# Performance work log

Hardware: AMD Instinct MI355X
Metric: run time of the kernel (lower is better)

## Reference

```python
import jax, jax.numpy as jnp
import numpy as np

DIM = 256      # dim_hidden * 2
HEADS = 8      # hier_tf_head
C = 256        # out_channels per head (concat=False)
FF = 1024      # dim_hidden * 8
N_HOPS = 4096
HOP_LEN = 12
N_MEM = N_HOPS * HOP_LEN
N = N_HOPS + N_MEM  # 53248 total nodes


def setup_inputs() -> dict:
    key = jax.random.key(0)
    ks = jax.random.split(key, 8)
    x = jax.random.normal(ks[0], (N, DIM), jnp.float32)
    # hop_attn structure built by the python loops: [j,j] self-edges for hop
    # tokens, then one edge (member_node -> hop_token) per member.
    hop_self = np.stack([np.arange(N_HOPS), np.arange(N_HOPS)])
    mem_src = np.arange(N_HOPS, N)
    mem_dst = np.arange(N_MEM) // HOP_LEN
    edge_index = jnp.asarray(
        np.concatenate([hop_self, np.stack([mem_src, mem_dst])], axis=1),
        jnp.int32)  # [2, E]

    def init(k, shp, fan):
        return jax.random.normal(k, shp, jnp.float32) / np.sqrt(fan).astype(np.float32)

    return {
        "x": x,
        "edge_index": edge_index,
        "gat_W": init(ks[1], (DIM, HEADS * C), DIM),
        "gat_att_src": init(ks[2], (HEADS, C), C),
        "gat_att_dst": init(ks[3], (HEADS, C), C),
        "gat_bias": jnp.zeros((C,), jnp.float32),
        "ffn_W1": init(ks[4], (DIM, FF), DIM),
        "ffn_b1": jnp.zeros((FF,), jnp.float32),
        "ffn_W2": init(ks[5], (FF, DIM), FF),
        "ffn_b2": jnp.zeros((DIM,), jnp.float32),
        "ln1_g": jnp.ones((DIM,), jnp.float32),
        "ln1_b": jnp.zeros((DIM,), jnp.float32),
        "ln2_g": jnp.ones((DIM,), jnp.float32),
        "ln2_b": jnp.zeros((DIM,), jnp.float32),
    }


def _layer_norm(x, g, b, eps=1e-5):
    mu = jnp.mean(x, axis=-1, keepdims=True)
    var = jnp.mean(jnp.square(x - mu), axis=-1, keepdims=True)
    return (x - mu) * jax.lax.rsqrt(var + eps) * g + b


def _gat_conv(x, src, dst, W, att_src, att_dst, bias):
    # PyG GATConv, concat=False (mean over heads), negative_slope=0.2
    h = (x @ W).reshape(N, HEADS, C)                       # [N,H,C]
    a_s = jnp.einsum('nhc,hc->nh', h, att_src)             # [N,H]
    a_d = jnp.einsum('nhc,hc->nh', h, att_dst)
    e = jax.nn.leaky_relu(a_s[src] + a_d[dst], 0.2)        # [E,H]
    m = jax.ops.segment_max(e, dst, num_segments=N)        # per-dst softmax
    e = jnp.exp(e - m[dst])
    denom = jax.ops.segment_sum(e, dst, num_segments=N)
    alpha = e / (denom[dst] + 1e-16)                       # [E,H]
    agg = jax.ops.segment_sum(h[src] * alpha[:, :, None], dst, num_segments=N)
    return agg.mean(axis=1) + bias                         # [N,DIM]


def reference(x, edge_index, gat_W, gat_att_src, gat_att_dst, gat_bias,
              ffn_W1, ffn_b1, ffn_W2, ffn_b2, ln1_g, ln1_b, ln2_g, ln2_b):
    # GATConv adds self-loops for every node by default
    loops = jnp.arange(N, dtype=edge_index.dtype)
    src = jnp.concatenate([edge_index[0], loops])
    dst = jnp.concatenate([edge_index[1], loops])
    # GAT + residual + LN (dropout is identity at eval)
    g_out = _gat_conv(x, src, dst, gat_W, gat_att_src, gat_att_dst, gat_bias)
    x1 = _layer_norm(g_out + x, ln1_g, ln1_b)
    # FFN + residual + LN
    ff = jax.nn.relu(x1 @ ffn_W1 + ffn_b1) @ ffn_W2 + ffn_b2
    return _layer_norm(ff + x1, ln2_g, ln2_b)
```

## Files before the change

### kernel.cpp

```cpp
#include <hip/hip_runtime.h>
#include <cstdint>
#include <cstddef>

#define N_TOT   53248
#define N_HOPS  4096
#define HOP_LEN 12
#define NHEAD   8
#define FFD     1024
#define GLD     384

typedef __bf16 bf16x8 __attribute__((ext_vector_type(8)));
typedef float f32x4 __attribute__((ext_vector_type(4)));

__device__ __forceinline__ unsigned short f2bf(float f) {
    unsigned int u = __float_as_uint(f);
    u += 0x7FFFu + ((u >> 16) & 1u);
    return (unsigned short)(u >> 16);
}
__device__ __forceinline__ float bf2f(unsigned short b) {
    return __uint_as_float((unsigned int)b << 16);
}
__device__ __forceinline__ void gload16(const void* g, void* l) {
    __builtin_amdgcn_global_load_lds(
        (const __attribute__((address_space(1))) void*)g,
        (__attribute__((address_space(3))) void*)l, 16, 0, 0);
}

__global__ __launch_bounds__(256) void prep_w(
    const float* __restrict__ W, const float* __restrict__ att_s,
    const float* __restrict__ att_d, unsigned short* __restrict__ BcT)
{
    int d = blockIdx.x, c = threadIdx.x;
    int wave = c >> 6;
    __shared__ float ps4[4], pd4[4];
    float wm = 0.f;
    for (int h = 0; h < NHEAD; ++h) {
        float w = W[d * 2048 + h * 256 + c];
        wm += w;
        float ps = w * att_s[h * 256 + c];
        float pd = w * att_d[h * 256 + c];
        for (int o = 32; o > 0; o >>= 1) {
            ps += __shfl_xor(ps, o);
            pd += __shfl_xor(pd, o);
        }
        if ((c & 63) == 0) { ps4[wave] = ps; pd4[wave] = pd; }
        __syncthreads();
        if (c == 0) BcT[(256 + h) * 256 + d] = f2bf(ps4[0] + ps4[1] + ps4[2] + ps4[3]);
        if (c == 1) BcT[(264 + h) * 256 + d] = f2bf(pd4[0] + pd4[1] + pd4[2] + pd4[3]);
        __syncthreads();
    }
    BcT[c * 256 + d] = f2bf(wm * 0.125f);
}

__global__ __launch_bounds__(256) void tconv(
    const float* __restrict__ in, unsigned short* __restrict__ out,
    int IS, int OS, int in_zoff, int out_zoff)
{
    __shared__ float t[32][33];
    in  += (size_t)blockIdx.z * in_zoff;
    out += (size_t)blockIdx.z * out_zoff;
    int tx = threadIdx.x, ty = threadIdx.y;
    int c0 = blockIdx.x * 32, r0 = blockIdx.y * 32;
    #pragma unroll
    for (int k = 0; k < 4; ++k)
        t[ty + 8 * k][tx] = in[(size_t)(r0 + ty + 8 * k) * IS + c0 + tx];
    __syncthreads();
    #pragma unroll
    for (int k = 0; k < 4; ++k)
        out[(size_t)(c0 + ty + 8 * k) * OS + r0 + tx] = f2bf(t[tx][ty + 8 * k]);
}

__global__ __launch_bounds__(256) void cvt_bf16(
    const float* __restrict__ in, unsigned short* __restrict__ out, int n4)
{
    int i = blockIdx.x * 256 + threadIdx.x;
    if (i >= n4) return;
    float4 v = ((const float4*)in)[i];
    ushort4 o;
    o.x = f2bf(v.x); o.y = f2bf(v.y); o.z = f2bf(v.z); o.w = f2bf(v.w);
    ((ushort4*)out)[i] = o;
}

__global__ __launch_bounds__(256) void hop_z(
    const unsigned short* __restrict__ xb, const unsigned short* __restrict__ gb,
    unsigned short* __restrict__ z)
{
    int j = blockIdx.x, tid = threadIdx.x;
    __shared__ float xr[13][256];
    __shared__ float sm[NHEAD][13];
    __shared__ float walpha[NHEAD][13];
    __shared__ float mxs[NHEAD], invs[NHEAD];

    for (int i = tid; i < 13 * 32; i += 256) {
        int r = i >> 5, c8 = (i & 31) * 8;
        int src = (r == 0) ? j : (N_HOPS + j * HOP_LEN + r - 1);
        uint4 u = *(const uint4*)&xb[(size_t)src * 256 + c8];
        float4 lo, hi;
        lo.x = bf2f((unsigned short)(u.x & 0xFFFF)); lo.y = bf2f((unsigned short)(u.x >> 16));
        lo.z = bf2f((unsigned short)(u.y & 0xFFFF)); lo.w = bf2f((unsigned short)(u.y >> 16));
        hi.x = bf2f((unsigned short)(u.z & 0xFFFF)); hi.y = bf2f((unsigned short)(u.z >> 16));
        hi.z = bf2f((unsigned short)(u.w & 0xFFFF)); hi.w = bf2f((unsigned short)(u.w >> 16));
        *(float4*)&xr[r][c8] = lo;
        *(float4*)&xr[r][c8 + 4] = hi;
    }
    if (tid < NHEAD * 13) {
        int h = tid / 13, k = tid % 13;
        int src = (k == 0) ? j : (N_HOPS + j * HOP_LEN + k - 1);
        float ad = bf2f(gb[(size_t)j * GLD + 264 + h]);
        float v = bf2f(gb[(size_t)src * GLD + 256 + h]) + ad;
        sm[h][k] = v > 0.f ? v : 0.2f * v;
    }
    __syncthreads();
    if (tid < NHEAD) {
        int h = tid;
        float mx = sm[h][0];
        for (int k = 1; k < 13; ++k) mx = fmaxf(mx, sm[h][k]);
        float sum = 2.f * expf(sm[h][0] - mx);
        for (int k = 1; k < 13; ++k) sum += expf(sm[h][k] - mx);
        mxs[h] = mx;
        invs[h] = 0.125f / (sum + 1e-16f);
    }
    __syncthreads();
    if (tid < NHEAD * 13) {
        int h = tid / 13, k = tid % 13;
        walpha[h][k] = (k == 0 ? 2.f : 1.f) * expf(sm[h][k] - mxs[h]) * invs[h];
    }
    __syncthreads();
    for (int h = 0; h < NHEAD; ++h) {
        float acc = 0.f;
        #pragma unroll
        for (int r = 0; r < 13; ++r) acc += walpha[h][r] * xr[r][tid];
        z[((size_t)j * NHEAD + h) * 256 + tid] = f2bf(acc);
    }
}

template <int RELU, int OUT_BF16, int SWZ>
__global__ __launch_bounds__(256) void gemm_bt(
    const unsigned short* __restrict__ A, const unsigned short* __restrict__ BT,
    const float* __restrict__ bias, void* __restrict__ Cout,
    int M, int Nc, int K, int ldc)
{
    __shared__ __align__(16) unsigned short As[128 * 32];
    __shared__ __align__(16) unsigned short Bs[128 * 32];
    const int tid = threadIdx.x;
    const int l = tid & 63;
    int bm, bn;
    if (SWZ) {
        int lid = blockIdx.x + gridDim.x * blockIdx.y;
        int per = (gridDim.x * gridDim.y) >> 3;
        int wg = (lid & 7) * per + (lid >> 3);
        bm = (wg / gridDim.x) * 128;
        bn = (wg % gridDim.x) * 128;
    } else {
        bm = blockIdx.y * 128; bn = blockIdx.x * 128;
    }
    const int wm = ((tid >> 6) >> 1) * 64, wn = ((tid >> 6) & 1) * 64;

    const int r0 = tid >> 2, ke0 = (tid & 3) * 8;
    const int r1 = (256 + tid) >> 2, ke1 = ((256 + tid) & 3) * 8;
    const unsigned short* ga0 = A + (size_t)(bm + r0) * K + ke0;
    const unsigned short* ga1 = A + (size_t)(bm + r1) * K + ke1;
    const unsigned short* gb0 = BT + (size_t)(bn + r0) * K + ke0;
    const unsigned short* gb1 = BT + (size_t)(bn + r1) * K + ke1;

    f32x4 acc[4][4];
    #pragma unroll
    for (int m = 0; m < 4; ++m)
        #pragma unroll
        for (int n = 0; n < 4; ++n)
            acc[m][n] = (f32x4){0.f, 0.f, 0.f, 0.f};

    const int lrow = l & 15, lk8 = (l >> 4) * 8;

    for (int k0 = 0; k0 < K; k0 += 32) {
        gload16(ga0 + k0, &As[(size_t)tid * 8]);
        gload16(ga1 + k0, &As[(size_t)(256 + tid) * 8]);
        gload16(gb0 + k0, &Bs[(size_t)tid * 8]);
        gload16(gb1 + k0, &Bs[(size_t)(256 + tid) * 8]);
        __syncthreads();
        bf16x8 af[4], bfr[4];
        #pragma unroll
        for (int m = 0; m < 4; ++m)
            af[m] = *(const bf16x8*)&As[(wm + m * 16 + lrow) * 32 + lk8];
        #pragma unroll
        for (int n = 0; n < 4; ++n)
            bfr[n] = *(const bf16x8*)&Bs[(wn + n * 16 + lrow) * 32 + lk8];
        #pragma unroll
        for (int m = 0; m < 4; ++m)
            #pragma unroll
            for (int n = 0; n < 4; ++n)
                acc[m][n] = __builtin_amdgcn_mfma_f32_16x16x32_bf16(
                    af[m], bfr[n], acc[m][n], 0, 0, 0);
        __syncthreads();
    }

    const int orow = (l >> 4) * 4, ocol = l & 15;
    #pragma unroll
    for (int m = 0; m < 4; ++m) {
        int gr = bm + wm + m * 16 + orow;
        #pragma unroll
        for (int n = 0; n < 4; ++n) {
            int gc = bn + wn + n * 16 + ocol;
            float bv = bias[gc];
            #pragma unroll
            for (int r = 0; r < 4; ++r) {
                float v = acc[m][n][r] + bv;
                if (RELU) v = fmaxf(v, 0.f);
                if (OUT_BF16)
                    ((unsigned short*)Cout)[(size_t)(gr + r) * ldc + gc] = f2bf(v);
                else
                    ((float*)Cout)[(size_t)(gr + r) * ldc + gc] = v;
            }
        }
    }
}

__global__ __launch_bounds__(256) void gemm_bt_sk(
    const unsigned short* __restrict__ A, const unsigned short* __restrict__ BT,
    unsigned short* __restrict__ Cpart, int M, int Nc, int Ksl, int ldA)
{
    __shared__ __align__(16) unsigned short As[128 * 32];
    __shared__ __align__(16) unsigned short Bs[128 * 32];
    const int tid = threadIdx.x;
    const int l = tid & 63;
    const int bm = blockIdx.y * 128, bn = blockIdx.x * 128;
    const int koff = blockIdx.z * Ksl;
    const int wm = ((tid >> 6) >> 1) * 64, wn = ((tid >> 6) & 1) * 64;

    const int r0 = tid >> 2, ke0 = (tid & 3) * 8;
    const int r1 = (256 + tid) >> 2, ke1 = ((256 + tid) & 3) * 8;
    const unsigned short* ga0 = A + (size_t)(bm + r0) * ldA + koff + ke0;
    const unsigned short* ga1 = A + (size_t)(bm + r1) * ldA + koff + ke1;
    const unsigned short* gb0 = BT + (size_t)(bn + r0) * ldA + koff + ke0;
    const unsigned short* gb1 = BT + (size_t)(bn + r1) * ldA + koff + ke1;

    f32x4 acc[4][4];
    #pragma unroll
    for (int m = 0; m < 4; ++m)
        #pragma unroll
        for (int n = 0; n < 4; ++n)
            acc[m][n] = (f32x4){0.f, 0.f, 0.f, 0.f};

    const int lrow = l & 15, lk8 = (l >> 4) * 8;

    for (int k0 = 0; k0 < Ksl; k0 += 32) {
        gload16(ga0 + k0, &As[(size_t)tid * 8]);
        gload16(ga1 + k0, &As[(size_t)(256 + tid) * 8]);
        gload16(gb0 + k0, &Bs[(size_t)tid * 8]);
        gload16(gb1 + k0, &Bs[(size_t)(256 + tid) * 8]);
        __syncthreads();
        bf16x8 af[4], bfr[4];
        #pragma unroll
        for (int m = 0; m < 4; ++m)
            af[m] = *(const bf16x8*)&As[(wm + m * 16 + lrow) * 32 + lk8];
        #pragma unroll
        for (int n = 0; n < 4; ++n)
            bfr[n] = *(const bf16x8*)&Bs[(wn + n * 16 + lrow) * 32 + lk8];
        #pragma unroll
        for (int m = 0; m < 4; ++m)
            #pragma unroll
            for (int n = 0; n < 4; ++n)
                acc[m][n] = __builtin_amdgcn_mfma_f32_16x16x32_bf16(
                    af[m], bfr[n], acc[m][n], 0, 0, 0);
        __syncthreads();
    }

    unsigned short* Cp = Cpart + (size_t)blockIdx.z * M * Nc;
    const int orow = (l >> 4) * 4, ocol = l & 15;
    #pragma unroll
    for (int m = 0; m < 4; ++m) {
        int gr = bm + wm + m * 16 + orow;
        #pragma unroll
        for (int n = 0; n < 4; ++n) {
            int gc = bn + wn + n * 16 + ocol;
            #pragma unroll
            for (int r = 0; r < 4; ++r)
                Cp[(size_t)(gr + r) * Nc + gc] = f2bf(acc[m][n][r]);
        }
    }
}

__global__ __launch_bounds__(256) void red_hop(
    const unsigned short* __restrict__ P, const float* __restrict__ bias,
    unsigned short* __restrict__ gbuf)
{
    int i = blockIdx.x * 256 + threadIdx.x;
    int row = i >> 6, c4 = (i & 63) * 4;
    float4 s = { 0.f, 0.f, 0.f, 0.f };
    #pragma unroll
    for (int zz = 0; zz < 8; ++zz) {
        ushort4 u = *(const ushort4*)&P[(size_t)zz * N_HOPS * 256 + (size_t)row * 256 + c4];
        s.x += bf2f(u.x); s.y += bf2f(u.y); s.z += bf2f(u.z); s.w += bf2f(u.w);
    }
    float4 bv = *(const float4*)&bias[c4];
    ushort4 o;
    o.x = f2bf(s.x + bv.x); o.y = f2bf(s.y + bv.y);
    o.z = f2bf(s.z + bv.z); o.w = f2bf(s.w + bv.w);
    *(ushort4*)&gbuf[(size_t)row * GLD + c4] = o;
}

__global__ __launch_bounds__(256) void ln_add_bb(
    const unsigned short* __restrict__ a, const unsigned short* __restrict__ b,
    const float* __restrict__ g, const float* __restrict__ be,
    unsigned short* __restrict__ outp)
{
    int wave = threadIdx.x >> 6, lane = threadIdx.x & 63;
    int n = blockIdx.x * 4 + wave;
    ushort4 av = *(const ushort4*)&a[(size_t)n * GLD + lane * 4];
    ushort4 bv = ((const ushort4*)b)[(size_t)n * 64 + lane];
    float v[4];
    v[0] = bf2f(av.x) + bf2f(bv.x); v[1] = bf2f(av.y) + bf2f(bv.y);
    v[2] = bf2f(av.z) + bf2f(bv.z); v[3] = bf2f(av.w) + bf2f(bv.w);
    float s = v[0] + v[1] + v[2] + v[3];
    for (int o = 32; o > 0; o >>= 1) s += __shfl_xor(s, o);
    float mu = s * (1.f / 256.f);
    float q = 0.f;
    #pragma unroll
    for (int i = 0; i < 4; ++i) { float d = v[i] - mu; q += d * d; }
    for (int o = 32; o > 0; o >>= 1) q += __shfl_xor(q, o);
    float rstd = rsqrtf(q * (1.f / 256.f) + 1e-5f);
    int c = lane * 4;
    float4 gv = *(const float4*)&g[c];
    float4 bev = *(const float4*)&be[c];
    ushort4 o4;
    o4.x = f2bf((v[0] - mu) * rstd * gv.x + bev.x);
    o4.y = f2bf((v[1] - mu) * rstd * gv.y + bev.y);
    o4.z = f2bf((v[2] - mu) * rstd * gv.z + bev.z);
    o4.w = f2bf((v[3] - mu) * rstd * gv.w + bev.w);
    ((ushort4*)outp)[(size_t)n * 64 + lane] = o4;
}

__global__ __launch_bounds__(512) void ffn2_ln(
    const unsigned short* __restrict__ hid, const unsigned short* __restrict__ W2T,
    const float* __restrict__ b2, const unsigned short* __restrict__ x1b,
    const float* __restrict__ g2, const float* __restrict__ be2,
    float* __restrict__ out)
{
    __shared__ __align__(16) unsigned short As[128 * 32];
    __shared__ __align__(16) unsigned short Bs[256 * 32];
    __shared__ float lnS[128][4], lnQ[128][4], lnM[128], lnR[128];

    const int tid = threadIdx.x, l = tid & 63, wid = tid >> 6;
    const int wr = wid >> 2, wc = wid & 3;
    const int lrow = l & 15, lk8 = (l >> 4) * 8;
    const int lid = blockIdx.x;
    const int row0 = ((lid & 7) * (416 / 8) + (lid >> 3)) * 128;

    const unsigned short* ga  = hid + (size_t)(row0 + (tid >> 2)) * FFD + (tid & 3) * 8;
    const unsigned short* gb0 = W2T + (size_t)(tid >> 2) * FFD + (tid & 3) * 8;
    const unsigned short* gb1 = W2T + (size_t)((512 + tid) >> 2) * FFD + ((512 + tid) & 3) * 8;

    f32x4 acc[4][4];
    #pragma unroll
    for (int m = 0; m < 4; ++m)
        #pragma unroll
        for (int n = 0; n < 4; ++n)
            acc[m][n] = (f32x4){0.f, 0.f, 0.f, 0.f};

    for (int k0 = 0; k0 < FFD; k0 += 32) {
        gload16(ga + k0,  &As[(size_t)tid * 8]);
        gload16(gb0 + k0, &Bs[(size_t)tid * 8]);
        gload16(gb1 + k0, &Bs[(size_t)(512 + tid) * 8]);
        __syncthreads();
        bf16x8 af[4], bfr[4];
        #pragma unroll
        for (int m = 0; m < 4; ++m)
            af[m] = *(const bf16x8*)&As[(wr * 64 + m * 16 + lrow) * 32 + lk8];
        #pragma unroll
        for (int n = 0; n < 4; ++n)
            bfr[n] = *(const bf16x8*)&Bs[(wc * 64 + n * 16 + lrow) * 32 + lk8];
        #pragma unroll
        for (int m = 0; m < 4; ++m)
            #pragma unroll
            for (int n = 0; n < 4; ++n)
                acc[m][n] = __builtin_amdgcn_mfma_f32_16x16x32_bf16(
                    af[m], bfr[n], acc[m][n], 0, 0, 0);
        __syncthreads();
    }

    const int orow = (l >> 4) * 4, ocol = l & 15;
    float b2c[4], g2c[4], be2c[4];
    #pragma unroll
    for (int n = 0; n < 4; ++n) {
        int col = wc * 64 + n * 16 + ocol;
        b2c[n] = b2[col]; g2c[n] = g2[col]; be2c[n] = be2[col];
    }
    #pragma unroll
    for (int m = 0; m < 4; ++m)
        #pragma unroll
        for (int r = 0; r < 4; ++r) {
            int row = wr * 64 + m * 16 + orow + r;
            #pragma unroll
            for (int n = 0; n < 4; ++n) {
                int col = wc * 64 + n * 16 + ocol;
                float res = bf2f(x1b[(size_t)(row0 + row) * 256 + col]);
                acc[m][n][r] += b2c[n] + res;
            }
        }
    #pragma unroll
    for (int m = 0; m < 4; ++m)
        #pragma unroll
        for (int r = 0; r < 4; ++r) {
            float s = 0.f, q = 0.f;
            #pragma unroll
            for (int n = 0; n < 4; ++n) {
                float v = acc[m][n][r];
                s += v; q += v * v;
            }
            #pragma unroll
            for (int o = 8; o >= 1; o >>= 1) {
                s += __shfl_xor(s, o);
                q += __shfl_xor(q, o);
            }
            if (ocol == 0) {
                int row = wr * 64 + m * 16 + orow + r;
                lnS[row][wc] = s; lnQ[row][wc] = q;
            }
        }
    __syncthreads();
    if (tid < 128) {
        float s = lnS[tid][0] + lnS[tid][1] + lnS[tid][2] + lnS[tid][3];
        float q = lnQ[tid][0] + lnQ[tid][1] + lnQ[tid][2] + lnQ[tid][3];
        float mu = s * (1.f / 256.f);
        lnM[tid] = mu;
        lnR[tid] = rsqrtf(q * (1.f / 256.f) - mu * mu + 1e-5f);
    }
    __syncthreads();
    #pragma unroll
    for (int m = 0; m < 4; ++m)
        #pragma unroll
        for (int r = 0; r < 4; ++r) {
            int row = wr * 64 + m * 16 + orow + r;
            float mu = lnM[row], rs = lnR[row];
            #pragma unroll
            for (int n = 0; n < 4; ++n) {
                int col = wc * 64 + n * 16 + ocol;
                out[(size_t)(row0 + row) * 256 + col] =
                    (acc[m][n][r] - mu) * rs * g2c[n] + be2c[n];
            }
        }
}

extern "C" void kernel_launch(void* const* d_in, const int* in_sizes, int n_in,
                              void* d_out, int out_size, void* d_ws, size_t ws_size,
                              hipStream_t stream)
{
    const float* x       = (const float*)d_in[0];
    const float* gat_W   = (const float*)d_in[2];
    const float* att_src = (const float*)d_in[3];
    const float* att_dst = (const float*)d_in[4];
    const float* gat_b   = (const float*)d_in[5];
    const float* W1      = (const float*)d_in[6];
    const float* b1      = (const float*)d_in[7];
    const float* W2      = (const float*)d_in[8];
    const float* b2      = (const float*)d_in[9];
    const float* ln1_g   = (const float*)d_in[10];
    const float* ln1_b   = (const float*)d_in[11];
    const float* ln2_g   = (const float*)d_in[12];
    const float* ln2_b   = (const float*)d_in[13];
    float* out = (float*)d_out;

    char* p = (char*)d_ws;
    auto carve = [&p](size_t bytes) { char* r = p; p += (bytes + 255) & ~(size_t)255; return r; };
    unsigned short* gbuf = (unsigned short*)carve((size_t)N_TOT * GLD * 2);
    unsigned short* x1b  = (unsigned short*)carve((size_t)N_TOT * 256 * 2);
    unsigned short* z    = (unsigned short*)carve((size_t)N_HOPS * 2048 * 2);
    unsigned short* hopP = (unsigned short*)carve((size_t)8 * N_HOPS * 256 * 2);
    unsigned short* hid  = (unsigned short*)carve((size_t)N_TOT * FFD * 2);
    unsigned short* BcT  = (unsigned short*)carve((size_t)GLD * 256 * 2);
    unsigned short* B2T  = (unsigned short*)carve((size_t)2048 * 256 * 2);
    unsigned short* W1T  = (unsigned short*)carve((size_t)FFD * 256 * 2);
    unsigned short* W2T  = (unsigned short*)carve((size_t)256 * FFD * 2);
    float*          bias384 = (float*)carve(GLD * 4);

    hipMemsetAsync(BcT + 272 * 256, 0, (size_t)(GLD - 272) * 256 * 2, stream);
    hipMemcpyAsync(bias384, gat_b, 256 * 4, hipMemcpyDeviceToDevice, stream);
    hipMemsetAsync(bias384 + 256, 0, (GLD - 256) * 4, stream);
    hipLaunchKernelGGL(prep_w, dim3(256), dim3(256), 0, stream,
                       gat_W, att_src, att_dst, BcT);
    hipLaunchKernelGGL(tconv, dim3(8, 8, 8), dim3(32, 8), 0, stream,
                       gat_W, B2T, 2048, 2048, 256, 256);
    hipLaunchKernelGGL(tconv, dim3(32, 8, 1), dim3(32, 8), 0, stream,
                       W1, W1T, 1024, 256, 0, 0);
    hipLaunchKernelGGL(tconv, dim3(8, 32, 1), dim3(32, 8), 0, stream,
                       W2, W2T, 256, 1024, 0, 0);
    hipLaunchKernelGGL(cvt_bf16, dim3(N_TOT * 256 / 4 / 256), dim3(256), 0, stream,
                       x, x1b, N_TOT * 256 / 4);
    hipLaunchKernelGGL((gemm_bt<0, 1, 1>), dim3(GLD / 128, N_TOT / 128), dim3(256), 0, stream,
                       x1b, BcT, bias384, gbuf, N_TOT, GLD, 256, GLD);
    hipLaunchKernelGGL(hop_z, dim3(N_HOPS), dim3(256), 0, stream,
                       x1b, gbuf, z);
    hipLaunchKernelGGL(gemm_bt_sk, dim3(2, N_HOPS / 128, 8), dim3(256), 0, stream,
                       z, B2T, hopP, N_HOPS, 256, 256, 2048);
    hipLaunchKernelGGL(red_hop, dim3(N_HOPS * 64 / 256), dim3(256), 0, stream,
                       hopP, gat_b, gbuf);
    hipLaunchKernelGGL(ln_add_bb, dim3(N_TOT / 4), dim3(256), 0, stream,
                       gbuf, x1b, ln1_g, ln1_b, x1b);
    hipLaunchKernelGGL((gemm_bt<1, 1, 1>), dim3(FFD / 128, N_TOT / 128), dim3(256), 0, stream,
                       x1b, W1T, b1, hid, N_TOT, FFD, 256, FFD);
    hipLaunchKernelGGL(ffn2_ln, dim3(N_TOT / 128), dim3(512), 0, stream,
                       hid, W2T, b2, x1b, ln2_g, ln2_b, out);
    (void)in_sizes; (void)n_in; (void)out_size; (void)ws_size;
}
```

Baseline: 239.8 us.

## Load GEMM operands directly into registers with double buffering instead of LDS

Replaces the LDS-staged tile loading (global_load_lds plus two barriers per k-step) in the main GEMMs and the fused FFN2+LayerNorm kernel with direct per-wave global loads into register fragments, double-buffered across k-steps of 32. This removes LDS traffic and block-wide synchronisation, and overlaps the next fragment loads with the current MFMAs. The cost is that operands shared between waves are no longer reused through LDS, so each wave re-reads A/B rows from global/L2 with strided 16-byte accesses, which raises cache traffic and register pressure.

```diff
diff --git a/kernel.cpp b/kernel.cpp
--- a/kernel.cpp
+++ b/kernel.cpp
@@ -134,34 +134,33 @@
     }
 }
 
-template <int RELU, int OUT_BF16, int SWZ>
-__global__ __launch_bounds__(256) void gemm_bt(
+#define MFMA16(AA, BB)                                                        \
+    _Pragma("unroll")                                                         \
+    for (int m = 0; m < 4; ++m) {                                             \
+        _Pragma("unroll")                                                     \
+        for (int n = 0; n < 4; ++n)                                           \
+            acc[m][n] = __builtin_amdgcn_mfma_f32_16x16x32_bf16(              \
+                AA[m], BB[n], acc[m][n], 0, 0, 0);                            \
+    }
+
+template <int RELU, int OUT_BF16>
+__global__ __launch_bounds__(256) void gemm_reg(
     const unsigned short* __restrict__ A, const unsigned short* __restrict__ BT,
     const float* __restrict__ bias, void* __restrict__ Cout,
     int M, int Nc, int K, int ldc)
 {
-    __shared__ __align__(16) unsigned short As[128 * 32];
-    __shared__ __align__(16) unsigned short Bs[128 * 32];
-    const int tid = threadIdx.x;
-    const int l = tid & 63;
-    int bm, bn;
-    if (SWZ) {
-        int lid = blockIdx.x + gridDim.x * blockIdx.y;
-        int per = (gridDim.x * gridDim.y) >> 3;
-        int wg = (lid & 7) * per + (lid >> 3);
-        bm = (wg / gridDim.x) * 128;
-        bn = (wg % gridDim.x) * 128;
-    } else {
-        bm = blockIdx.y * 128; bn = blockIdx.x * 128;
-    }
+    const int tid = threadIdx.x, l = tid & 63;
+    const int lid = blockIdx.x + gridDim.x * blockIdx.y;
+    const int per = (gridDim.x * gridDim.y) >> 3;
+    const int wg = (lid & 7) * per + (lid >> 3);
+    const int bm = (wg / gridDim.x) * 128;
+    const int bn = (wg % gridDim.x) * 128;
     const int wm = ((tid >> 6) >> 1) * 64, wn = ((tid >> 6) & 1) * 64;
-
-    const int r0 = tid >> 2, ke0 = (tid & 3) * 8;
-    const int r1 = (256 + tid) >> 2, ke1 = ((256 + tid) & 3) * 8;
-    const unsigned short* ga0 = A + (size_t)(bm + r0) * K + ke0;
-    const unsigned short* ga1 = A + (size_t)(bm + r1) * K + ke1;
-    const unsigned short* gb0 = BT + (size_t)(bn + r0) * K + ke0;
-    const unsigned short* gb1 = BT + (size_t)(bn + r1) * K + ke1;
+    const int lrow = l & 15, lk8 = (l >> 4) * 8;
+
+    const unsigned short* pa = A + (size_t)(bm + wm + lrow) * K + lk8;
+    const unsigned short* pb = BT + (size_t)(bn + wn + lrow) * K + lk8;
+    const size_t mK = (size_t)16 * K;
 
     f32x4 acc[4][4];
     #pragma unroll
@@ -170,28 +169,25 @@
         for (int n = 0; n < 4; ++n)
             acc[m][n] = (f32x4){0.f, 0.f, 0.f, 0.f};
 
-    const int lrow = l & 15, lk8 = (l >> 4) * 8;
-
-    for (int k0 = 0; k0 < K; k0 += 32) {
-        gload16(ga0 + k0, &As[(size_t)tid * 8]);
-        gload16(ga1 + k0, &As[(size_t)(256 + tid) * 8]);
-        gload16(gb0 + k0, &Bs[(size_t)tid * 8]);
-        gload16(gb1 + k0, &Bs[(size_t)(256 + tid) * 8]);
-        __syncthreads();
-        bf16x8 af[4], bfr[4];
-        #pragma unroll
-        for (int m = 0; m < 4; ++m)
-            af[m] = *(const bf16x8*)&As[(wm + m * 16 + lrow) * 32 + lk8];
-        #pragma unroll
-        for (int n = 0; n < 4; ++n)
-            bfr[n] = *(const bf16x8*)&Bs[(wn + n * 16 + lrow) * 32 + lk8];
-        #pragma unroll
-        for (int m = 0; m < 4; ++m)
-            #pragma unroll
-            for (int n = 0; n < 4; ++n)
-                acc[m][n] = __builtin_amdgcn_mfma_f32_16x16x32_bf16(
-                    af[m], bfr[n], acc[m][n], 0, 0, 0);
-        __syncthreads();
+    bf16x8 a0[4], b0[4], a1[4], b1[4];
+    #pragma unroll
+    for (int m = 0; m < 4; ++m) a0[m] = *(const bf16x8*)(pa + m * mK);
+    #pragma unroll
+    for (int n = 0; n < 4; ++n) b0[n] = *(const bf16x8*)(pb + n * mK);
+
+    for (int k = 0; k < K; k += 64) {
+        #pragma unroll
+        for (int m = 0; m < 4; ++m) a1[m] = *(const bf16x8*)(pa + k + 32 + m * mK);
+        #pragma unroll
+        for (int n = 0; n < 4; ++n) b1[n] = *(const bf16x8*)(pb + k + 32 + n * mK);
+        MFMA16(a0, b0);
+        if (k + 64 < K) {
+            #pragma unroll
+            for (int m = 0; m < 4; ++m) a0[m] = *(const bf16x8*)(pa + k + 64 + m * mK);
+            #pragma unroll
+            for (int n = 0; n < 4; ++n) b0[n] = *(const bf16x8*)(pb + k + 64 + n * mK);
+        }
+        MFMA16(a1, b1);
     }
 
     const int orow = (l >> 4) * 4, ocol = l & 15;
@@ -336,19 +332,17 @@
     const float* __restrict__ g2, const float* __restrict__ be2,
     float* __restrict__ out)
 {
-    __shared__ __align__(16) unsigned short As[128 * 32];
-    __shared__ __align__(16) unsigned short Bs[256 * 32];
     __shared__ float lnS[128][4], lnQ[128][4], lnM[128], lnR[128];
 
     const int tid = threadIdx.x, l = tid & 63, wid = tid >> 6;
     const int wr = wid >> 2, wc = wid & 3;
     const int lrow = l & 15, lk8 = (l >> 4) * 8;
     const int lid = blockIdx.x;
-    const int row0 = ((lid & 7) * (416 / 8) + (lid >> 3)) * 128;
-
-    const unsigned short* ga  = hid + (size_t)(row0 + (tid >> 2)) * FFD + (tid & 3) * 8;
-    const unsigned short* gb0 = W2T + (size_t)(tid >> 2) * FFD + (tid & 3) * 8;
-    const unsigned short* gb1 = W2T + (size_t)((512 + tid) >> 2) * FFD + ((512 + tid) & 3) * 8;
+    const int row0 = ((lid & 7) * 52 + (lid >> 3)) * 128;
+
+    const unsigned short* pa = hid + (size_t)(row0 + wr * 64 + lrow) * FFD + lk8;
+    const unsigned short* pb = W2T + (size_t)(wc * 64 + lrow) * FFD + lk8;
+    const size_t mK = (size_t)16 * FFD;
 
     f32x4 acc[4][4];
     #pragma unroll
@@ -357,25 +351,25 @@
         for (int n = 0; n < 4; ++n)
             acc[m][n] = (f32x4){0.f, 0.f, 0.f, 0.f};
 
-    for (int k0 = 0; k0 < FFD; k0 += 32) {
-        gload16(ga + k0,  &As[(size_t)tid * 8]);
-        gload16(gb0 + k0, &Bs[(size_t)tid * 8]);
-        gload16(gb1 + k0, &Bs[(size_t)(512 + tid) * 8]);
-        __syncthreads();
-        bf16x8 af[4], bfr[4];
-        #pragma unroll
-        for (int m = 0; m < 4; ++m)
-            af[m] = *(const bf16x8*)&As[(wr * 64 + m * 16 + lrow) * 32 + lk8];
-        #pragma unroll
-        for (int n = 0; n < 4; ++n)
-            bfr[n] = *(const bf16x8*)&Bs[(wc * 64 + n * 16 + lrow) * 32 + lk8];
-        #pragma unroll
-        for (int m = 0; m < 4; ++m)
-            #pragma unroll
-            for (int n = 0; n < 4; ++n)
-                acc[m][n] = __builtin_amdgcn_mfma_f32_16x16x32_bf16(
-                    af[m], bfr[n], acc[m][n], 0, 0, 0);
-        __syncthreads();
+    bf16x8 a0[4], b0[4], a1[4], b1[4];
+    #pragma unroll
+    for (int m = 0; m < 4; ++m) a0[m] = *(const bf16x8*)(pa + m * mK);
+    #pragma unroll
+    for (int n = 0; n < 4; ++n) b0[n] = *(const bf16x8*)(pb + n * mK);
+
+    for (int k = 0; k < FFD; k += 64) {
+        #pragma unroll
+        for (int m = 0; m < 4; ++m) a1[m] = *(const bf16x8*)(pa + k + 32 + m * mK);
+        #pragma unroll
+        for (int n = 0; n < 4; ++n) b1[n] = *(const bf16x8*)(pb + k + 32 + n * mK);
+        MFMA16(a0, b0);
+        if (k + 64 < FFD) {
+            #pragma unroll
+            for (int m = 0; m < 4; ++m) a0[m] = *(const bf16x8*)(pa + k + 64 + m * mK);
+            #pragma unroll
+            for (int n = 0; n < 4; ++n) b0[n] = *(const bf16x8*)(pb + k + 64 + n * mK);
+        }
+        MFMA16(a1, b1);
     }
 
     const int orow = (l >> 4) * 4, ocol = l & 15;
@@ -486,7 +480,7 @@
                        W2, W2T, 256, 1024, 0, 0);
     hipLaunchKernelGGL(cvt_bf16, dim3(N_TOT * 256 / 4 / 256), dim3(256), 0, stream,
                        x, x1b, N_TOT * 256 / 4);
-    hipLaunchKernelGGL((gemm_bt<0, 1, 1>), dim3(GLD / 128, N_TOT / 128), dim3(256), 0, stream,
+    hipLaunchKernelGGL((gemm_reg<0, 1>), dim3(GLD / 128, N_TOT / 128), dim3(256), 0, stream,
                        x1b, BcT, bias384, gbuf, N_TOT, GLD, 256, GLD);
     hipLaunchKernelGGL(hop_z, dim3(N_HOPS), dim3(256), 0, stream,
                        x1b, gbuf, z);
@@ -496,7 +490,7 @@
                        hopP, gat_b, gbuf);
     hipLaunchKernelGGL(ln_add_bb, dim3(N_TOT / 4), dim3(256), 0, stream,
                        gbuf, x1b, ln1_g, ln1_b, x1b);
-    hipLaunchKernelGGL((gemm_bt<1, 1, 1>), dim3(FFD / 128, N_TOT / 128), dim3(256), 0, stream,
+    hipLaunchKernelGGL((gemm_reg<1, 1>), dim3(FFD / 128, N_TOT / 128), dim3(256), 0, stream,
                        x1b, W1T, b1, hid, N_TOT, FFD, 256, FFD);
     hipLaunchKernelGGL(ffn2_ln, dim3(N_TOT / 128), dim3(512), 0, stream,
                        hid, W2T, b2, x1b, ln2_g, ln2_b, out);
```

Result: slower. 379.6 us (+58.3%).
